# Kernel tuning notes

Hardware: AMD Instinct MI355X
Metric: run time of the kernel (lower is better)

Reference implementation:

```python
import jax, jax.numpy as jnp
import numpy as np

N_L = 100000   # local nodes
N_V = 1000     # virtual nodes
D_IN = 64
H = 64         # hidden_channels
D_OUT = 32
E_LL = 1000000
E_LV = 100000
E_VV = 50000


def setup_inputs() -> dict:
    key = jax.random.key(0)
    ks = jax.random.split(key, 16)
    s_in = 1.0 / np.sqrt(D_IN)   # fan-in init scale
    s_h = 1.0 / np.sqrt(H)
    return {
        "x_local": jax.random.normal(ks[0], (N_L, D_IN), jnp.float32),
        "x_virtual": jax.random.normal(ks[1], (N_V, D_IN), jnp.float32),
        # GCNConv (local->local): weight + bias
        "W_gcn": jax.random.normal(ks[2], (D_IN, H), jnp.float32) * s_in,
        "b_gcn": jnp.zeros((H,), jnp.float32),
        # SAGEConv (local->virtual): lin_l (neighbor agg, with bias), lin_r (root)
        "Wl_lv": jax.random.normal(ks[3], (D_IN, H), jnp.float32) * s_in,
        "Wr_lv": jax.random.normal(ks[4], (D_IN, H), jnp.float32) * s_in,
        "b_lv": jnp.zeros((H,), jnp.float32),
        # SAGEConv (virtual->virtual)
        "Wl_vv": jax.random.normal(ks[5], (D_IN, H), jnp.float32) * s_in,
        "Wr_vv": jax.random.normal(ks[6], (D_IN, H), jnp.float32) * s_in,
        "b_vv": jnp.zeros((H,), jnp.float32),
        # final Linear(hidden -> dim_out)
        "W_lin": jax.random.normal(ks[7], (H, D_OUT), jnp.float32) * s_h,
        "b_lin": jnp.zeros((D_OUT,), jnp.float32),
        # edge indices
        "edge_ll": jax.random.randint(ks[8], (2, E_LL), 0, N_L),
        "edge_lv_src": jax.random.randint(ks[9], (E_LV,), 0, N_L),
        "edge_lv_dst": jax.random.randint(ks[10], (E_LV,), 0, N_V),
        "edge_vv": jax.random.randint(ks[11], (2, E_VV), 0, N_V),
    }


def _gcn_conv(x, W, b, row, col, n):
    # gcn_norm with add_self_loops=False: deg from dst (col), sym norm
    ones = jnp.ones(row.shape[0], x.dtype)
    deg = jax.ops.segment_sum(ones, col, num_segments=n)
    dinv = jnp.where(deg > 0, jax.lax.rsqrt(jnp.maximum(deg, 1.0)), 0.0)
    norm = dinv[row] * dinv[col]                      # [E]
    h = x @ W                                         # [n,H]
    msg = h[row] * norm[:, None]                      # [E,H] gather
    return jax.ops.segment_sum(msg, col, num_segments=n) + b


def _sage_conv(x_src, x_dst, Wl, Wr, b, src, dst, n_dst):
    # mean aggregation of source features over in-edges
    agg = jax.ops.segment_sum(x_src[src], dst, num_segments=n_dst)
    cnt = jax.ops.segment_sum(jnp.ones(src.shape[0], x_src.dtype), dst,
                              num_segments=n_dst)
    agg = agg / jnp.maximum(cnt, 1.0)[:, None]
    return agg @ Wl + b + x_dst @ Wr


def reference(x_local, x_virtual, W_gcn, b_gcn, Wl_lv, Wr_lv, b_lv,
              Wl_vv, Wr_vv, b_vv, W_lin, b_lin,
              edge_ll, edge_lv_src, edge_lv_dst, edge_vv):
    # HeteroConv layer (sum-aggregate outputs per destination node type)
    out_ll = _gcn_conv(x_local, W_gcn, b_gcn, edge_ll[0], edge_ll[1], N_L)
    out_lv = _sage_conv(x_local, x_virtual, Wl_lv, Wr_lv, b_lv,
                        edge_lv_src, edge_lv_dst, N_V)
    out_vv = _sage_conv(x_virtual, x_virtual, Wl_vv, Wr_vv, b_vv,
                        edge_vv[0], edge_vv[1], N_V)
    h_local = jax.nn.relu(out_ll)
    h_virtual = jax.nn.relu(out_lv + out_vv)  # sum across relations -> relu
    del h_virtual  # only 'local' feeds the final linear head
    return h_local @ W_lin + b_lin
```

## Files before the change

kernel.cpp:

```cpp
#include <hip/hip_runtime.h>

#define N_L 100000
#define N_V 1000
#define D_IN 64
#define HCH 64
#define D_OUT 32
#define E_LL 1000000

#define NCLS 8
#define DST_PER_CLS 12500
#define NBLK1 1024
#define BCAP 256
#define GW 400
#define HW 200
#define NSB 32
#define NGSB 256
#define SUBCAP 4608
#define SORTCAP 2560
#define SCSTRIDE 16

#define L2CAP 384
#define L2THR 128
#define BINSUB_BPC 64
#define SLABS (NBLK1 / BINSUB_BPC)

typedef unsigned int uint32;
typedef unsigned long long u64;
typedef __attribute__((ext_vector_type(8))) short bfx8;
typedef __attribute__((ext_vector_type(4))) float f32x4;
typedef __attribute__((ext_vector_type(4))) float fvec4;
typedef __attribute__((ext_vector_type(4))) unsigned short usvec4;

__device__ inline float bf2f(unsigned short u) {
    return __uint_as_float(((uint32)u) << 16);
}
__device__ inline unsigned short f2bf(float f) {
    uint32 u = __float_as_uint(f);
    u = (u + 0x7fffu + ((u >> 16) & 1u)) >> 16;
    return (unsigned short)u;
}
__device__ inline void bar_lds() {
    asm volatile("s_waitcnt lgkmcnt(0)\n\ts_barrier" ::: "memory");
}

__global__ __launch_bounds__(256) void binclass_kernel(
    const int* __restrict__ row, const int* __restrict__ col,
    int* __restrict__ classcnt, uint32* __restrict__ classpairs)
{
    __shared__ uint32 sbin[NCLS][BCAP];
    __shared__ int scnt[NCLS];
    if (threadIdx.x < NCLS) scnt[threadIdx.x] = 0;
    bar_lds();

    const int blk = blockIdx.x;
    const int per = (E_LL + NBLK1 - 1) / NBLK1;
    const int beg = blk * per;
    const int end = (beg + per < E_LL) ? beg + per : E_LL;
    const int lane = threadIdx.x & 63;
    const int wv = threadIdx.x >> 6;

    for (int i0 = beg; i0 < end; i0 += 256) {
        int i = i0 + threadIdx.x;
        if (i < end) {
            int c = col[i];
            int r = row[i];
            int cls = c / DST_PER_CLS;
            uint32 pack = ((uint32)r << 14) | (uint32)(c - cls * DST_PER_CLS);
            u64 act = __ballot(1);
            u64 b0 = __ballot(cls & 1);
            u64 b1 = __ballot(cls & 2);
            u64 b2 = __ballot(cls & 4);
            u64 mask = ((cls & 1) ? b0 : ~b0) & ((cls & 2) ? b1 : ~b1)
                     & ((cls & 4) ? b2 : ~b2) & act;
            int leader = __ffsll(mask) - 1;
            int rank = __popcll(mask & ((1ull << lane) - 1ull));
            int base = 0;
            if (lane == leader) base = atomicAdd(&scnt[cls], __popcll(mask));
            base = __shfl(base, leader);
            int slot = base + rank;
            if (slot < BCAP) sbin[cls][slot] = pack;
        }
    }
    bar_lds();
    for (int b = wv; b < NCLS; b += 4) {
        int cnt = scnt[b]; if (cnt > BCAP) cnt = BCAP;
        uint32* dst = classpairs + ((size_t)b * NBLK1 + blk) * BCAP;
        for (int k = lane; k < cnt; k += 64) dst[k] = sbin[b][k];
        if (lane == 0) classcnt[b * NBLK1 + blk] = cnt;
    }
}

__global__ __launch_bounds__(256) void binsub_kernel(
    const int* __restrict__ classcnt, const uint32* __restrict__ classpairs,
    int* __restrict__ subcur, uint32* __restrict__ subpairs)
{
    __shared__ uint32 sbin[NSB][L2CAP];
    __shared__ int scnt[NSB];
    if (threadIdx.x < NSB) scnt[threadIdx.x] = 0;
    bar_lds();

    const int cls = blockIdx.x / BINSUB_BPC;
    const int chunk = blockIdx.x % BINSUB_BPC;
    const int s0 = chunk * SLABS;
    const int lane = threadIdx.x & 63;
    const int wv = threadIdx.x >> 6;

    for (int s = s0; s < s0 + SLABS; ++s) {
        int len = classcnt[cls * NBLK1 + s];
        const uint32* cp = classpairs + ((size_t)cls * NBLK1 + s) * BCAP;
        if (threadIdx.x < len) {
            uint32 p = cp[threadIdx.x];
            int c_lo = (int)(p & 16383u);
            uint32 r = p >> 14;
            int sb = c_lo / GW;
            uint32 pack = (r << 9) | (uint32)(c_lo - sb * GW);
            u64 act = __ballot(1);
            u64 b0 = __ballot(sb & 1);
            u64 b1 = __ballot(sb & 2);
            u64 b2 = __ballot(sb & 4);
            u64 b3 = __ballot(sb & 8);
            u64 b4 = __ballot(sb & 16);
            u64 mask = ((sb & 1) ? b0 : ~b0) & ((sb & 2) ? b1 : ~b1)
                     & ((sb & 4) ? b2 : ~b2) & ((sb & 8) ? b3 : ~b3)
                     & ((sb & 16) ? b4 : ~b4) & act;
            int leader = __ffsll(mask) - 1;
            int rank = __popcll(mask & ((1ull << lane) - 1ull));
            int base = 0;
            if (lane == leader) base = atomicAdd(&scnt[sb], __popcll(mask));
            base = __shfl(base, leader);
            sbin[sb][base + rank] = pack;
        }
        bar_lds();
        for (int b = wv; b < NSB; b += 4) {
            int cnt = scnt[b];
            if (cnt >= L2THR) {
                int gb;
                int gsb = cls * NSB + b;
                if (lane == 0) gb = atomicAdd(&subcur[gsb * SCSTRIDE], cnt);
                gb = __shfl(gb, 0);
                uint32* dst = subpairs + (size_t)gsb * SUBCAP;
                for (int k = lane; k < cnt; k += 64)
                    if (gb + k < SUBCAP) dst[gb + k] = sbin[b][k];
                if (lane == 0) scnt[b] = 0;
            }
        }
        bar_lds();
    }
    for (int b = wv; b < NSB; b += 4) {
        int cnt = scnt[b];
        if (cnt > 0) {
            int gb;
            int gsb = cls * NSB + b;
            if (lane == 0) gb = atomicAdd(&subcur[gsb * SCSTRIDE], cnt);
            gb = __shfl(gb, 0);
            uint32* dst = subpairs + (size_t)gsb * SUBCAP;
            for (int k = lane; k < cnt; k += 64)
                if (gb + k < SUBCAP) dst[gb + k] = sbin[b][k];
        }
    }
}

__global__ __launch_bounds__(512) void degdinv_kernel(
    const uint32* __restrict__ subpairs, const int* __restrict__ subcur,
    float* __restrict__ dinv)
{
    __shared__ int hcnt[512];
    const int gsb = blockIdx.x;
    const int cls = gsb >> 5;
    const int sb = gsb & 31;
    const int lo = cls * DST_PER_CLS + sb * GW;
    int w = DST_PER_CLS - sb * GW; if (w > GW) w = GW;

    hcnt[threadIdx.x] = 0;
    bar_lds();
    int cnt = subcur[gsb * SCSTRIDE]; if (cnt > SUBCAP) cnt = SUBCAP;
    const uint32* sp = subpairs + (size_t)gsb * SUBCAP;
    for (int i = threadIdx.x; i < cnt; i += 512)
        atomicAdd(&hcnt[sp[i] & 511u], 1);
    bar_lds();
    if (threadIdx.x < w) {
        int d = hcnt[threadIdx.x];
        dinv[lo + threadIdx.x] = (d > 0) ? rsqrtf((float)d) : 0.0f;
    }
}

__global__ void xbconv_kernel(const float* __restrict__ x,
                              const float* __restrict__ dinv,
                              unsigned short* __restrict__ xb) {
    int n4 = N_L * D_IN / 4;
    int idx = blockIdx.x * blockDim.x + threadIdx.x;
    int stride = gridDim.x * blockDim.x;
    for (; idx < n4; idx += stride) {
        fvec4 v = ((const fvec4*)x)[idx];
        float d = dinv[idx >> 4];
        usvec4 o;
        o.x = f2bf(v.x * d);
        o.y = f2bf(v.y * d);
        o.z = f2bf(v.z * d);
        o.w = f2bf(v.w * d);
        ((usvec4*)xb)[idx] = o;
    }
}

__global__ __launch_bounds__(512) void gather_epi_kernel(
    const unsigned short* __restrict__ xb,
    const uint32* __restrict__ subpairs, const int* __restrict__ subcur,
    const float* __restrict__ Wg, const float* __restrict__ bg,
    const float* __restrict__ Wl, const float* __restrict__ bl,
    float* __restrict__ out)
{
    extern __shared__ char smem[];
    unsigned short* hacc  = (unsigned short*)smem;
    unsigned short* hbufp = (unsigned short*)(smem + 29952);
    uint32* sorted = (uint32*)(smem + 48384);
    int* hist  = (int*)(smem + 58624);
    int* scn   = (int*)(smem + 59648);
    int* cur   = (int*)(smem + 60672);
    float* bpart = (float*)(smem + 61696);
    int* bnode = (int*)(smem + 65792);

    const int gsb = blockIdx.x >> 1;
    const int hb  = blockIdx.x & 1;
    const int cls = gsb >> 5;
    const int sb  = gsb & 31;
    const int lo_bin = cls * DST_PER_CLS + sb * GW;
    int wbin = DST_PER_CLS - sb * GW; if (wbin > GW) wbin = GW;
    const int lo_node = hb * HW;
    int w = wbin - lo_node; if (w > HW) w = HW; if (w < 0) w = 0;
    const int lo = lo_bin + lo_node;

    const int tid = threadIdx.x;
    const int lane = tid & 63;
    const int wv = tid >> 6;

    int cnt = subcur[gsb * SCSTRIDE]; if (cnt > SUBCAP) cnt = SUBCAP;
    const uint32* sp = subpairs + (size_t)gsb * SUBCAP;

    {
        uint32* hz = (uint32*)hacc;
        for (int i = tid; i < 208 * 36; i += 512) hz[i] = 0u;
        if (tid < 256) hist[tid] = 0;
        if (tid < 16) bnode[tid] = -1;
    }
    bar_lds();

    for (int i = tid; i < cnt; i += 512) {
        int cl = (int)(sp[i] & 511u) - lo_node;
        if (cl >= 0 && cl < w) atomicAdd(&hist[cl], 1);
    }
    bar_lds();

    int v = (tid < 256) ? hist[tid] : 0;
    if (tid < 256) scn[tid] = v;
    bar_lds();
    for (int ofs = 1; ofs < 256; ofs <<= 1) {
        int add = (tid < 256 && tid >= ofs) ? scn[tid - ofs] : 0;
        bar_lds();
        if (tid < 256) scn[tid] += add;
        bar_lds();
    }
    if (tid < 256) cur[tid] = scn[tid] - v;
    bar_lds();

    for (int i = tid; i < cnt; i += 512) {
        uint32 p = sp[i];
        int cl = (int)(p & 511u) - lo_node;
        if (cl >= 0 && cl < w) {
            int pos = atomicAdd(&cur[cl], 1);
            if (pos < SORTCAP) sorted[pos] = ((p >> 9) << 8) | (uint32)cl;
        }
    }
    bar_lds();

    int ch = scn[255]; if (ch > SORTCAP) ch = SORTCAP;
    {
        int a = (ch * wv) >> 3;
        int b = (ch * (wv + 1)) >> 3;
        if (a < b) {
            float acc = 0.0f;
            int curn = (int)(sorted[a] & 255u);
            bool firstopen = true;

#define GSTEP(EK, VK)                                                        \
            {                                                                \
                int nk = (int)((EK) & 255u);                                 \
                if (nk != curn) {                                            \
                    if (firstopen) {                                         \
                        bpart[(2 * wv) * 64 + lane] = acc;                   \
                        if (lane == 0) bnode[2 * wv] = curn;                 \
                        firstopen = false;                                   \
                    } else {                                                 \
                        hacc[curn * 72 + lane] =                             \
                            f2bf(acc * rsqrtf((float)hist[curn]));           \
                    }                                                        \
                    acc = 0.0f; curn = nk;                                   \
                }                                                            \
                acc += (VK);                                                 \
            }

            int j = a;
            for (; j + 8 <= b; j += 8) {
                uint32 e0 = sorted[j + 0], e1 = sorted[j + 1];
                uint32 e2 = sorted[j + 2], e3 = sorted[j + 3];
                uint32 e4 = sorted[j + 4], e5 = sorted[j + 5];
                uint32 e6 = sorted[j + 6], e7 = sorted[j + 7];
                float v0 = bf2f(xb[(size_t)(e0 >> 8) * D_IN + lane]);
                float v1 = bf2f(xb[(size_t)(e1 >> 8) * D_IN + lane]);
                float v2 = bf2f(xb[(size_t)(e2 >> 8) * D_IN + lane]);
                float v3 = bf2f(xb[(size_t)(e3 >> 8) * D_IN + lane]);
                float v4 = bf2f(xb[(size_t)(e4 >> 8) * D_IN + lane]);
                float v5 = bf2f(xb[(size_t)(e5 >> 8) * D_IN + lane]);
                float v6 = bf2f(xb[(size_t)(e6 >> 8) * D_IN + lane]);
                float v7 = bf2f(xb[(size_t)(e7 >> 8) * D_IN + lane]);
                GSTEP(e0, v0) GSTEP(e1, v1) GSTEP(e2, v2) GSTEP(e3, v3)
                GSTEP(e4, v4) GSTEP(e5, v5) GSTEP(e6, v6) GSTEP(e7, v7)
            }
            for (; j < b; ++j) {
                uint32 e = sorted[j];
                float vv = bf2f(xb[(size_t)(e >> 8) * D_IN + lane]);
                GSTEP(e, vv)
            }
#undef GSTEP
            if (firstopen) {
                bpart[(2 * wv) * 64 + lane] = acc;
                if (lane == 0) bnode[2 * wv] = curn;
            } else {
                bpart[(2 * wv + 1) * 64 + lane] = acc;
                if (lane == 0) bnode[2 * wv + 1] = curn;
            }
        }
    }
    bar_lds();

    if (wv == 0) {
        for (int e2 = 0; e2 < 16; ++e2) {
            int n = bnode[e2];
            if (n < 0) continue;
            bool first = true;
            for (int f = 0; f < e2; ++f)
                if (bnode[f] == n) { first = false; break; }
            if (!first) continue;
            float s = bpart[e2 * 64 + lane];
            for (int f = e2 + 1; f < 16; ++f)
                if (bnode[f] == n) s += bpart[f * 64 + lane];
            hacc[n * 72 + lane] = f2bf(s * rsqrtf((float)hist[n]));
        }
    }
    bar_lds();

    if (w == 0) return;

    const int lm = lane & 15, lg = lane >> 4, kseg = lg * 8;

    bfx8 wg0[4], wg1[4], wl0[2], wl1[2];
    #pragma unroll
    for (int n = 0; n < 4; ++n) {
        #pragma unroll
        for (int jj = 0; jj < 8; ++jj) {
            wg0[n][jj] = (short)f2bf(Wg[(kseg + jj) * HCH + n * 16 + lm]);
            wg1[n][jj] = (short)f2bf(Wg[(32 + kseg + jj) * HCH + n * 16 + lm]);
        }
    }
    #pragma unroll
    for (int n = 0; n < 2; ++n) {
        #pragma unroll
        for (int jj = 0; jj < 8; ++jj) {
            wl0[n][jj] = (short)f2bf(Wl[(kseg + jj) * D_OUT + n * 16 + lm]);
            wl1[n][jj] = (short)f2bf(Wl[(32 + kseg + jj) * D_OUT + n * 16 + lm]);
        }
    }
    float bgv[4], blv[2];
    #pragma unroll
    for (int n = 0; n < 4; ++n) bgv[n] = bg[n * 16 + lm];
    #pragma unroll
    for (int n = 0; n < 2; ++n) blv[n] = bl[n * 16 + lm];

    const int ntile = (w + 15) >> 4;
    for (int t = wv; t < ntile; t += 8) {
        const int m0 = t * 16;
        const int arow = m0 + lm;
        const unsigned short* fr = hacc + arow * 72;
        bfx8 a0 = *(const bfx8*)(fr + kseg);
        bfx8 a1 = *(const bfx8*)(fr + 32 + kseg);

        unsigned short* hbw = hbufp + wv * (16 * 72);
        #pragma unroll
        for (int n = 0; n < 4; ++n) {
            f32x4 cacc = {0.0f, 0.0f, 0.0f, 0.0f};
            cacc = __builtin_amdgcn_mfma_f32_16x16x32_bf16(a0, wg0[n], cacc, 0, 0, 0);
            cacc = __builtin_amdgcn_mfma_f32_16x16x32_bf16(a1, wg1[n], cacc, 0, 0, 0);
            #pragma unroll
            for (int i = 0; i < 4; ++i) {
                float h = fmaxf(cacc[i] + bgv[n], 0.0f);
                hbw[(lg * 4 + i) * 72 + n * 16 + lm] = f2bf(h);
            }
        }
        bfx8 a20 = *(const bfx8*)(hbw + lm * 72 + kseg);
        bfx8 a21 = *(const bfx8*)(hbw + lm * 72 + 32 + kseg);

        #pragma unroll
        for (int n2 = 0; n2 < 2; ++n2) {
            f32x4 d = {0.0f, 0.0f, 0.0f, 0.0f};
            d = __builtin_amdgcn_mfma_f32_16x16x32_bf16(a20, wl0[n2], d, 0, 0, 0);
            d = __builtin_amdgcn_mfma_f32_16x16x32_bf16(a21, wl1[n2], d, 0, 0, 0);
            #pragma unroll
            for (int i = 0; i < 4; ++i) {
                int mrow = m0 + lg * 4 + i;
                if (mrow < w)
                    out[(size_t)(lo + mrow) * D_OUT + n2 * 16 + lm] = d[i] + blv[n2];
            }
        }
    }
}

extern "C" void kernel_launch(void* const* d_in, const int* in_sizes, int n_in,
                              void* d_out, int out_size, void* d_ws, size_t ws_size,
                              hipStream_t stream) {
    const float* x_local = (const float*)d_in[0];
    const float* W_gcn   = (const float*)d_in[2];
    const float* b_gcn   = (const float*)d_in[3];
    const float* W_lin   = (const float*)d_in[10];
    const float* b_lin   = (const float*)d_in[11];
    const int*   edge_ll = (const int*)d_in[12];
    const int*   row = edge_ll;
    const int*   col = edge_ll + E_LL;

    char* base = (char*)d_ws;
    int*    subcur     = (int*)(base + 0);
    int*    classcnt   = (int*)(base + 16384);
    float*  dinvp      = (float*)(base + 49152);
    uint32* classpairs = (uint32*)(base + 449536);
    uint32* subpairs   = (uint32*)(base + 8838144);
    unsigned short* xb = (unsigned short*)(base + 13556736);
    float* out = (float*)d_out;

    (void)hipMemsetAsync(base, 0, 16384, stream);

    binclass_kernel<<<NBLK1, 256, 0, stream>>>(row, col, classcnt, classpairs);
    binsub_kernel<<<NCLS * BINSUB_BPC, 256, 0, stream>>>(
        classcnt, classpairs, subcur, subpairs);
    degdinv_kernel<<<NGSB, 512, 0, stream>>>(subpairs, subcur, dinvp);
    xbconv_kernel<<<2048, 256, 0, stream>>>(x_local, dinvp, xb);
    gather_epi_kernel<<<2 * NGSB, 512, 65856, stream>>>(
        xb, subpairs, subcur, W_gcn, b_gcn, W_lin, b_lin, out);
}
```

Before: 100.7 us.

## Split gather into 32 quarter-wave slices with vector bf16 loads and shuffle scan

The gather loop now has each 16-lane quarter-wave own its own contiguous slice of sorted edges, so each wave handles 4 slices. Each lane loads 4 bf16 features with one vector load, where before one wave walked one slice with a scalar load per lane. The LDS-based Hillis-Steele prefix scan, with its many barriers, becomes a wave-level shuffle scan plus a small per-wave sum combine. Boundary partials grow from 16 to 64 slots and their merge is spread across all waves. LDS use rises from about 64 KB to about 76 KB, which may lower occupancy, and the boundary merge does more redundant work.

After: 135.2 us. 34.2% more time.

```diff
diff --git a/kernel.cpp b/kernel.cpp
--- a/kernel.cpp
+++ b/kernel.cpp
@@ -214,10 +214,10 @@
     unsigned short* hbufp = (unsigned short*)(smem + 29952);
     uint32* sorted = (uint32*)(smem + 48384);
     int* hist  = (int*)(smem + 58624);
-    int* scn   = (int*)(smem + 59648);
-    int* cur   = (int*)(smem + 60672);
-    float* bpart = (float*)(smem + 61696);
-    int* bnode = (int*)(smem + 65792);
+    int* cur   = (int*)(smem + 59648);
+    float* bpart = (float*)(smem + 60672);
+    int* bnode = (int*)(smem + 77056);
+    int* wsum  = (int*)(smem + 77312);
 
     const int gsb = blockIdx.x >> 1;
     const int hb  = blockIdx.x & 1;
@@ -232,6 +232,8 @@
     const int tid = threadIdx.x;
     const int lane = tid & 63;
     const int wv = tid >> 6;
+    const int lq = lane >> 4;
+    const int fl = lane & 15;
 
     int cnt = subcur[gsb * SCSTRIDE]; if (cnt > SUBCAP) cnt = SUBCAP;
     const uint32* sp = subpairs + (size_t)gsb * SUBCAP;
@@ -240,7 +242,8 @@
         uint32* hz = (uint32*)hacc;
         for (int i = tid; i < 208 * 36; i += 512) hz[i] = 0u;
         if (tid < 256) hist[tid] = 0;
-        if (tid < 16) bnode[tid] = -1;
+        if (tid < 64) bnode[tid] = -1;
+        if (tid < 8) wsum[tid] = 0;
     }
     bar_lds();
 
@@ -251,15 +254,21 @@
     bar_lds();
 
     int v = (tid < 256) ? hist[tid] : 0;
-    if (tid < 256) scn[tid] = v;
-    bar_lds();
-    for (int ofs = 1; ofs < 256; ofs <<= 1) {
-        int add = (tid < 256 && tid >= ofs) ? scn[tid - ofs] : 0;
-        bar_lds();
-        if (tid < 256) scn[tid] += add;
-        bar_lds();
-    }
-    if (tid < 256) cur[tid] = scn[tid] - v;
+    int x = v;
+    #pragma unroll
+    for (int ofs = 1; ofs < 64; ofs <<= 1) {
+        int t = __shfl_up(x, ofs, 64);
+        if (lane >= ofs) x += t;
+    }
+    if (tid < 256 && lane == 63) wsum[wv] = x;
+    bar_lds();
+    int ch = wsum[0] + wsum[1] + wsum[2] + wsum[3];
+    if (ch > SORTCAP) ch = SORTCAP;
+    if (tid < 256) {
+        int pref = 0;
+        for (int k = 0; k < wv; ++k) pref += wsum[k];
+        cur[tid] = x - v + pref;
+    }
     bar_lds();
 
     for (int i = tid; i < cnt; i += 512) {
@@ -272,79 +281,89 @@
     }
     bar_lds();
 
-    int ch = scn[255]; if (ch > SORTCAP) ch = SORTCAP;
     {
-        int a = (ch * wv) >> 3;
-        int b = (ch * (wv + 1)) >> 3;
-        if (a < b) {
-            float acc = 0.0f;
-            int curn = (int)(sorted[a] & 255u);
-            bool firstopen = true;
-
-#define GSTEP(EK, VK)                                                        \
-            {                                                                \
-                int nk = (int)((EK) & 255u);                                 \
-                if (nk != curn) {                                            \
-                    if (firstopen) {                                         \
-                        bpart[(2 * wv) * 64 + lane] = acc;                   \
-                        if (lane == 0) bnode[2 * wv] = curn;                 \
-                        firstopen = false;                                   \
-                    } else {                                                 \
-                        hacc[curn * 72 + lane] =                             \
-                            f2bf(acc * rsqrtf((float)hist[curn]));           \
-                    }                                                        \
-                    acc = 0.0f; curn = nk;                                   \
-                }                                                            \
-                acc += (VK);                                                 \
+        const int sl = (wv << 2) | lq;
+        const int a = (ch * sl) >> 5;
+        const int b = (ch * (sl + 1)) >> 5;
+        const int bs0 = 2 * sl, bs1 = 2 * sl + 1;
+        float ac0 = 0.f, ac1 = 0.f, ac2 = 0.f, ac3 = 0.f;
+        int curn = -1;
+        bool firstopen = true;
+
+#define FLUSHCUR()                                                          \
+        {                                                                   \
+            if (firstopen) {                                                \
+                fvec4 bv = {ac0, ac1, ac2, ac3};                            \
+                *(fvec4*)(bpart + bs0 * 64 + fl * 4) = bv;                  \
+                if (fl == 0) bnode[bs0] = curn;                             \
+                firstopen = false;                                          \
+            } else {                                                        \
+                float dv = rsqrtf((float)hist[curn]);                       \
+                usvec4 o;                                                   \
+                o.x = f2bf(ac0 * dv); o.y = f2bf(ac1 * dv);                 \
+                o.z = f2bf(ac2 * dv); o.w = f2bf(ac3 * dv);                 \
+                *(usvec4*)(hacc + curn * 72 + fl * 4) = o;                  \
+            }                                                               \
+        }
+#define GSTEP(EK, VK)                                                       \
+        {                                                                   \
+            int nk = (int)((EK) & 255u);                                    \
+            if (nk != curn) {                                               \
+                if (curn >= 0) FLUSHCUR();                                  \
+                ac0 = ac1 = ac2 = ac3 = 0.f; curn = nk;                     \
+            }                                                               \
+            ac0 += bf2f((VK).x); ac1 += bf2f((VK).y);                       \
+            ac2 += bf2f((VK).z); ac3 += bf2f((VK).w);                       \
+        }
+
+        int j = a;
+        for (; j + 8 <= b; j += 8) {
+            uint32 e0 = sorted[j + 0], e1 = sorted[j + 1];
+            uint32 e2 = sorted[j + 2], e3 = sorted[j + 3];
+            uint32 e4 = sorted[j + 4], e5 = sorted[j + 5];
+            uint32 e6 = sorted[j + 6], e7 = sorted[j + 7];
+            usvec4 v0 = *(const usvec4*)(xb + ((size_t)(e0 >> 8) << 6) + (fl << 2));
+            usvec4 v1 = *(const usvec4*)(xb + ((size_t)(e1 >> 8) << 6) + (fl << 2));
+            usvec4 v2 = *(const usvec4*)(xb + ((size_t)(e2 >> 8) << 6) + (fl << 2));
+            usvec4 v3 = *(const usvec4*)(xb + ((size_t)(e3 >> 8) << 6) + (fl << 2));
+            usvec4 v4 = *(const usvec4*)(xb + ((size_t)(e4 >> 8) << 6) + (fl << 2));
+            usvec4 v5 = *(const usvec4*)(xb + ((size_t)(e5 >> 8) << 6) + (fl << 2));
+            usvec4 v6 = *(const usvec4*)(xb + ((size_t)(e6 >> 8) << 6) + (fl << 2));
+            usvec4 v7 = *(const usvec4*)(xb + ((size_t)(e7 >> 8) << 6) + (fl << 2));
+            GSTEP(e0, v0) GSTEP(e1, v1) GSTEP(e2, v2) GSTEP(e3, v3)
+            GSTEP(e4, v4) GSTEP(e5, v5) GSTEP(e6, v6) GSTEP(e7, v7)
+        }
+        for (; j < b; ++j) {
+            uint32 e = sorted[j];
+            usvec4 vv = *(const usvec4*)(xb + ((size_t)(e >> 8) << 6) + (fl << 2));
+            GSTEP(e, vv)
+        }
+        if (curn >= 0) {
+            fvec4 bv = {ac0, ac1, ac2, ac3};
+            if (firstopen) {
+                *(fvec4*)(bpart + bs0 * 64 + fl * 4) = bv;
+                if (fl == 0) bnode[bs0] = curn;
+            } else {
+                *(fvec4*)(bpart + bs1 * 64 + fl * 4) = bv;
+                if (fl == 0) bnode[bs1] = curn;
             }
-
-            int j = a;
-            for (; j + 8 <= b; j += 8) {
-                uint32 e0 = sorted[j + 0], e1 = sorted[j + 1];
-                uint32 e2 = sorted[j + 2], e3 = sorted[j + 3];
-                uint32 e4 = sorted[j + 4], e5 = sorted[j + 5];
-                uint32 e6 = sorted[j + 6], e7 = sorted[j + 7];
-                float v0 = bf2f(xb[(size_t)(e0 >> 8) * D_IN + lane]);
-                float v1 = bf2f(xb[(size_t)(e1 >> 8) * D_IN + lane]);
-                float v2 = bf2f(xb[(size_t)(e2 >> 8) * D_IN + lane]);
-                float v3 = bf2f(xb[(size_t)(e3 >> 8) * D_IN + lane]);
-                float v4 = bf2f(xb[(size_t)(e4 >> 8) * D_IN + lane]);
-                float v5 = bf2f(xb[(size_t)(e5 >> 8) * D_IN + lane]);
-                float v6 = bf2f(xb[(size_t)(e6 >> 8) * D_IN + lane]);
-                float v7 = bf2f(xb[(size_t)(e7 >> 8) * D_IN + lane]);
-                GSTEP(e0, v0) GSTEP(e1, v1) GSTEP(e2, v2) GSTEP(e3, v3)
-                GSTEP(e4, v4) GSTEP(e5, v5) GSTEP(e6, v6) GSTEP(e7, v7)
-            }
-            for (; j < b; ++j) {
-                uint32 e = sorted[j];
-                float vv = bf2f(xb[(size_t)(e >> 8) * D_IN + lane]);
-                GSTEP(e, vv)
-            }
+        }
 #undef GSTEP
-            if (firstopen) {
-                bpart[(2 * wv) * 64 + lane] = acc;
-                if (lane == 0) bnode[2 * wv] = curn;
-            } else {
-                bpart[(2 * wv + 1) * 64 + lane] = acc;
-                if (lane == 0) bnode[2 * wv + 1] = curn;
-            }
-        }
-    }
-    bar_lds();
-
-    if (wv == 0) {
-        for (int e2 = 0; e2 < 16; ++e2) {
-            int n = bnode[e2];
-            if (n < 0) continue;
-            bool first = true;
-            for (int f = 0; f < e2; ++f)
-                if (bnode[f] == n) { first = false; break; }
-            if (!first) continue;
-            float s = bpart[e2 * 64 + lane];
-            for (int f = e2 + 1; f < 16; ++f)
-                if (bnode[f] == n) s += bpart[f * 64 + lane];
-            hacc[n * 72 + lane] = f2bf(s * rsqrtf((float)hist[n]));
-        }
+#undef FLUSHCUR
+    }
+    bar_lds();
+
+    for (int e2 = wv; e2 < 64; e2 += 8) {
+        int n = bnode[e2];
+        if (n < 0) continue;
+        bool lead = true;
+        for (int f = 0; f < e2; ++f)
+            if (bnode[f] == n) { lead = false; break; }
+        if (!lead) continue;
+        float s = bpart[e2 * 64 + lane];
+        for (int f = e2 + 1; f < 64; ++f)
+            if (bnode[f] == n) s += bpart[f * 64 + lane];
+        hacc[n * 72 + lane] = f2bf(s * rsqrtf((float)hist[n]));
     }
     bar_lds();
 
@@ -441,6 +460,6 @@
         classcnt, classpairs, subcur, subpairs);
     degdinv_kernel<<<NGSB, 512, 0, stream>>>(subpairs, subcur, dinvp);
     xbconv_kernel<<<2048, 256, 0, stream>>>(x_local, dinvp, xb);
-    gather_epi_kernel<<<2 * NGSB, 512, 65856, stream>>>(
+    gather_epi_kernel<<<2 * NGSB, 512, 77376, stream>>>(
         xb, subpairs, subcur, W_gcn, b_gcn, W_lin, b_lin, out);
 }
```

## Fuse degree/dinv computation into bf16 scaling kernel and halve binning slab size

Applied to the files above, without the earlier changes.

Merges the degree-histogram/dinv kernel with the x-to-bf16 scaling kernel, so each sub-bin block computes dinv in LDS and then scales its own 400 rows of x. This removes one launch and the global dinv round trip. The first binning pass now uses twice as many blocks with half the per-slab capacity, and binsub processes two slabs per iteration, using 128 threads per slab. The scaling work is now limited to 256 blocks, which may lower parallelism for the streaming conversion. The smaller BCAP also risks overflow if a class slab exceeds 128 entries.

After: 101.1 us. About the same (+0.3%).

```diff
diff --git a/kernel.cpp b/kernel.cpp
--- a/kernel.cpp
+++ b/kernel.cpp
@@ -9,8 +9,8 @@
 
 #define NCLS 8
 #define DST_PER_CLS 12500
-#define NBLK1 1024
-#define BCAP 256
+#define NBLK1 2048
+#define BCAP 128
 #define GW 400
 #define HW 200
 #define NSB 32
@@ -55,7 +55,7 @@
     const int blk = blockIdx.x;
     const int per = (E_LL + NBLK1 - 1) / NBLK1;
     const int beg = blk * per;
-    const int end = (beg + per < E_LL) ? beg + per : E_LL;
+    int end = beg + per; if (end > E_LL) end = E_LL;
     const int lane = threadIdx.x & 63;
     const int wv = threadIdx.x >> 6;
 
@@ -105,11 +105,12 @@
     const int lane = threadIdx.x & 63;
     const int wv = threadIdx.x >> 6;
 
-    for (int s = s0; s < s0 + SLABS; ++s) {
-        int len = classcnt[cls * NBLK1 + s];
-        const uint32* cp = classpairs + ((size_t)cls * NBLK1 + s) * BCAP;
-        if (threadIdx.x < len) {
-            uint32 p = cp[threadIdx.x];
+    for (int sr = 0; sr < SLABS; sr += 2) {
+        int sA = s0 + sr + (threadIdx.x >> 7);
+        int idx = threadIdx.x & 127;
+        int len = classcnt[cls * NBLK1 + sA];
+        if (idx < len) {
+            uint32 p = classpairs[((size_t)cls * NBLK1 + sA) * BCAP + idx];
             int c_lo = (int)(p & 16383u);
             uint32 r = p >> 14;
             int sb = c_lo / GW;
@@ -160,45 +161,45 @@
     }
 }
 
-__global__ __launch_bounds__(512) void degdinv_kernel(
+__global__ __launch_bounds__(512) void xbscale_kernel(
     const uint32* __restrict__ subpairs, const int* __restrict__ subcur,
-    float* __restrict__ dinv)
+    const float* __restrict__ x, unsigned short* __restrict__ xb)
 {
     __shared__ int hcnt[512];
+    __shared__ float sdinv[GW];
     const int gsb = blockIdx.x;
     const int cls = gsb >> 5;
     const int sb = gsb & 31;
     const int lo = cls * DST_PER_CLS + sb * GW;
     int w = DST_PER_CLS - sb * GW; if (w > GW) w = GW;
-
-    hcnt[threadIdx.x] = 0;
+    const int tid = threadIdx.x;
+
+    hcnt[tid] = 0;
     bar_lds();
     int cnt = subcur[gsb * SCSTRIDE]; if (cnt > SUBCAP) cnt = SUBCAP;
     const uint32* sp = subpairs + (size_t)gsb * SUBCAP;
-    for (int i = threadIdx.x; i < cnt; i += 512)
+    for (int i = tid; i < cnt; i += 512)
         atomicAdd(&hcnt[sp[i] & 511u], 1);
     bar_lds();
-    if (threadIdx.x < w) {
-        int d = hcnt[threadIdx.x];
-        dinv[lo + threadIdx.x] = (d > 0) ? rsqrtf((float)d) : 0.0f;
-    }
-}
-
-__global__ void xbconv_kernel(const float* __restrict__ x,
-                              const float* __restrict__ dinv,
-                              unsigned short* __restrict__ xb) {
-    int n4 = N_L * D_IN / 4;
-    int idx = blockIdx.x * blockDim.x + threadIdx.x;
-    int stride = gridDim.x * blockDim.x;
-    for (; idx < n4; idx += stride) {
-        fvec4 v = ((const fvec4*)x)[idx];
-        float d = dinv[idx >> 4];
+    if (tid < w) {
+        int d = hcnt[tid];
+        sdinv[tid] = (d > 0) ? rsqrtf((float)d) : 0.0f;
+    }
+    bar_lds();
+
+    const fvec4* x4 = (const fvec4*)x;
+    usvec4* xb4 = (usvec4*)xb;
+    const int total = w * 16;
+    for (int i = tid; i < total; i += 512) {
+        int r = i >> 4;
+        fvec4 v = x4[(size_t)(lo + r) * 16 + (i & 15)];
+        float d = sdinv[r];
         usvec4 o;
         o.x = f2bf(v.x * d);
         o.y = f2bf(v.y * d);
         o.z = f2bf(v.z * d);
         o.w = f2bf(v.w * d);
-        ((usvec4*)xb)[idx] = o;
+        xb4[(size_t)(lo + r) * 16 + (i & 15)] = o;
     }
 }
 
@@ -428,10 +429,9 @@
     char* base = (char*)d_ws;
     int*    subcur     = (int*)(base + 0);
     int*    classcnt   = (int*)(base + 16384);
-    float*  dinvp      = (float*)(base + 49152);
-    uint32* classpairs = (uint32*)(base + 449536);
-    uint32* subpairs   = (uint32*)(base + 8838144);
-    unsigned short* xb = (unsigned short*)(base + 13556736);
+    uint32* classpairs = (uint32*)(base + 81920);
+    uint32* subpairs   = (uint32*)(base + 8470528);
+    unsigned short* xb = (unsigned short*)(base + 13189120);
     float* out = (float*)d_out;
 
     (void)hipMemsetAsync(base, 0, 16384, stream);
@@ -439,8 +439,7 @@
     binclass_kernel<<<NBLK1, 256, 0, stream>>>(row, col, classcnt, classpairs);
     binsub_kernel<<<NCLS * BINSUB_BPC, 256, 0, stream>>>(
         classcnt, classpairs, subcur, subpairs);
-    degdinv_kernel<<<NGSB, 512, 0, stream>>>(subpairs, subcur, dinvp);
-    xbconv_kernel<<<2048, 256, 0, stream>>>(x_local, dinvp, xb);
+    xbscale_kernel<<<NGSB, 512, 0, stream>>>(subpairs, subcur, x_local, xb);
     gather_epi_kernel<<<2 * NGSB, 512, 65856, stream>>>(
         xb, subpairs, subcur, W_gcn, b_gcn, W_lin, b_lin, out);
 }
```
